# Performance work log

Measured on AMD Instinct MI355X. Metric: run time of the kernel, lower is better.

Reference implementation:

```python
import jax, jax.numpy as jnp
import numpy as np

B, L, D = 32, 256, 128


def hard_sigmoid(x):
    # Keras-1 default inner_activation for LSTM gates
    return jnp.clip(0.2 * x + 0.5, 0.0, 1.0)


def lstm_step(x_t, h, c, W, U, b):
    # Keras-1 gate order: i, f, c(candidate), o
    z = x_t @ W + h @ U + b  # [B, 4D]
    d = h.shape[-1]
    i = hard_sigmoid(z[:, :d])
    f = hard_sigmoid(z[:, d:2 * d])
    g = jnp.tanh(z[:, 2 * d:3 * d])
    o = hard_sigmoid(z[:, 3 * d:])
    c_new = f * c + i * g
    h_new = o * jnp.tanh(c_new)
    return h_new, c_new


def setup_inputs() -> dict:
    key = jax.random.key(0)
    ks = jax.random.split(key, 9)
    s = 0.05  # weight scale to keep activations in a sane range
    return {
        "x": jax.random.normal(ks[0], (B, L, D), dtype=jnp.float32),
        "Wr": jax.random.normal(ks[1], (D, 4 * D), dtype=jnp.float32) * s,
        "Ur": jax.random.normal(ks[2], (D, 4 * D), dtype=jnp.float32) * s,
        "br": jnp.zeros((4 * D,), dtype=jnp.float32),
        "Ww": jax.random.normal(ks[3], (D, 4 * D), dtype=jnp.float32) * s,
        "Uw": jax.random.normal(ks[4], (D, 4 * D), dtype=jnp.float32) * s,
        "bw": jnp.zeros((4 * D,), dtype=jnp.float32),
        "Wc": jax.random.normal(ks[5], (2 * D, D), dtype=jnp.float32) * s,
        "bc": jnp.zeros((D,), dtype=jnp.float32),
    }


def reference(x, Wr, Ur, br, Ww, Uw, bw, Wc, bc):
    b, l, d = x.shape
    h0 = jnp.zeros((b, d), dtype=x.dtype)

    # ---- reader LSTM (return_sequences) ----
    def reader_step(carry, x_t):
        h, c = carry
        h, c = lstm_step(x_t, h, c, Wr, Ur, br)
        return (h, c), h

    _, o_seq = jax.lax.scan(reader_step, (h0, h0), jnp.swapaxes(x, 0, 1))  # [L, B, D]

    # ---- compose-and-write scan over timesteps ----
    mem0 = x  # read() sets mem_0 = input

    def write_step(carry, o_t):
        mem, h, c = carry  # mem: [B, L, D]
        # eq 2-3: attention over memory slots
        z = jax.nn.softmax(jnp.einsum('bd,bld->bl', o_t, mem), axis=-1)  # [B, L]
        m_rt = jnp.einsum('bl,bld->bd', z, mem)  # [B, D]
        # eq 4: composer (linear activation)
        c_t = jnp.concatenate([o_t, m_rt], axis=-1) @ Wc + bc  # [B, D]
        # eq 5: writer LSTM step
        h, c = lstm_step(c_t, h, c, Ww, Uw, bw)
        # eq 6: soft overwrite of memory
        zc = z[:, :, None]
        mem = mem * (1.0 - zc) + h[:, None, :] * zc
        return (mem, h, c), h

    (_, _, _), hs = jax.lax.scan(write_step, (mem0, h0, h0), o_seq)
    # return_mode == 'last_output'
    return hs[-1]
```

## Files before the change

kernel.cpp:

```cpp
#include <hip/hip_runtime.h>
#include <stdint.h>


#define LL 256

typedef float v2f __attribute__((ext_vector_type(2)));

__device__ __forceinline__ float hsig(float x) { return fminf(fmaxf(fmaf(x, 0.2f, 0.5f), 0.f), 1.f); }
__device__ __forceinline__ float tanh_fast(float x) {
  x = fminf(fmaxf(x, -15.f), 15.f);
  float e = __expf(2.f * x);
  return (e - 1.f) / (e + 1.f);
}

__global__ __launch_bounds__(512) void wtrans_kernel(const float* __restrict__ src,
                                                     float* __restrict__ dst, int jshift) {
  int idx = blockIdx.x * 512 + threadIdx.x;
  int J = 1 << jshift;
  int k = idx >> jshift, j = idx & (J - 1);
  dst[(((size_t)(k >> 2) << jshift) + j) * 4 + (k & 3)] = src[idx];
}

__global__ __launch_bounds__(512) void pvw_gemm(const float* __restrict__ Wc,
                                                const float* __restrict__ Ww,
                                                float* __restrict__ PVw) {
  __shared__ float wrow[128];
  const int r = blockIdx.x, j = threadIdx.x;
  if (j < 128) wrow[j] = Wc[r * 128 + j];
  __syncthreads();
  float a = 0.f;
#pragma unroll 4
  for (int m = 0; m < 128; m++) a = fmaf(wrow[m], Ww[m * 512 + j], a);
  PVw[r * 512 + j] = a;
}

__global__ __launch_bounds__(512) void pz_kernel(const float* __restrict__ bc,
                                                 const float* __restrict__ Ww,
                                                 const float* __restrict__ bw,
                                                 float* __restrict__ pz) {
  __shared__ float b_s[128];
  const int j = threadIdx.x;
  if (j < 128) b_s[j] = bc[j];
  __syncthreads();
  float a = bw[j];
#pragma unroll 4
  for (int m = 0; m < 128; m++) a = fmaf(b_s[m], Ww[m * 512 + j], a);
  pz[j] = a;
}

__global__ __launch_bounds__(512) void xw_gemm(const float* __restrict__ x,
                                               const float4* __restrict__ WrT4,
                                               const float* __restrict__ br,
                                               float* __restrict__ XW) {
  alignas(16) __shared__ float xs[8][128];
  const int b = blockIdx.x >> 5, tg = blockIdx.x & 31, tid = threadIdx.x;
  const float* xg = x + ((size_t)b * LL + tg * 8) * 128;
  if (tid < 256) ((float4*)&xs[0][0])[tid] = ((const float4*)xg)[tid];
  __syncthreads();
  float acc[8];
#pragma unroll
  for (int r = 0; r < 8; r++) acc[r] = 0.f;
#pragma unroll 8
  for (int i4 = 0; i4 < 32; i4++) {
    float4 w4 = WrT4[i4 * 512 + tid];
#pragma unroll
    for (int r = 0; r < 8; r++) {
      float4 v = *(const float4*)&xs[r][4 * i4];
      acc[r] += w4.x * v.x + w4.y * v.y + w4.z * v.z + w4.w * v.w;
    }
  }
  const float brj = br[tid];
  float* o = XW + ((size_t)b * LL + tg * 8) * 512;
#pragma unroll
  for (int r = 0; r < 8; r++) o[r * 512 + tid] = acc[r] + brj;
}

__global__ __launch_bounds__(512, 2) void reader_kernel(const float4* __restrict__ UrT4,
                                                        const float* __restrict__ XW,
                                                        float* __restrict__ og) {
  alignas(16) __shared__ float h_s[128];
  alignas(16) __shared__ float pp_s[512];
  const int b = blockIdx.x, tid = threadIdx.x;
  const float* XWb = XW + (size_t)b * LL * 512;
  float* ogb = og + (size_t)b * LL * 128;

  float4 U[32];
#pragma unroll
  for (int i4 = 0; i4 < 32; i4++) U[i4] = UrT4[i4 * 512 + tid];

  float c_r = 0.f;
  if (tid < 128) h_s[tid] = 0.f;
  float xwv = XWb[tid];
  __syncthreads();

  for (int t = 0; t < LL; t++) {
    float xw_n = (t + 1 < LL) ? XWb[(t + 1) * 512 + tid] : 0.f;
    v2f acc[4] = {{0.f, 0.f}, {0.f, 0.f}, {0.f, 0.f}, {0.f, 0.f}};
#pragma unroll
    for (int i4 = 0; i4 < 32; i4++) {
      float4 v = *(const float4*)&h_s[4 * i4];
      float4 w = U[i4];
      acc[i4 & 3] += (v2f){w.x, w.y} * (v2f){v.x, v.y};
      acc[i4 & 3] += (v2f){w.z, w.w} * (v2f){v.z, v.w};
    }
    v2f A = (acc[0] + acc[1]) + (acc[2] + acc[3]);
    pp_s[tid] = A.x + A.y + xwv;
    __syncthreads();
    if (tid < 128) {
      float zi = pp_s[tid], zf = pp_s[128 + tid], zg = pp_s[256 + tid], zo = pp_s[384 + tid];
      float ii = hsig(zi), ff = hsig(zf), gg = tanh_fast(zg), oo = hsig(zo);
      c_r = fmaf(ff, c_r, ii * gg);
      float h = oo * tanh_fast(c_r);
      h_s[tid] = h;
      ogb[t * 128 + tid] = h;
    }
    __syncthreads();
    xwv = xw_n;
  }
}

template <int NC>
__global__ __launch_bounds__(512, 2) void writer_kernel(
    const float* __restrict__ x,
    const float4* __restrict__ VwT4, const float4* __restrict__ UwT4,
    const float* __restrict__ og, const float* __restrict__ ZW,
    float* __restrict__ out) {
  alignas(16) __shared__ float h_s[128];
  alignas(16) __shared__ float osN[128];
  alignas(16) __shared__ float sc_s[256], ee_s[256];
  alignas(16) __shared__ float mr_s[128];
  alignas(16) __shared__ float pp_s[1024];
  __shared__ float rr_s[16];
  extern __shared__ float4 UwL[];

  const int b = blockIdx.x, tid = threadIdx.x;
  const int lane = tid & 63, wv = tid >> 6;
  const int l = tid >> 1, hf = tid & 1;
  const int q = tid >> 6, dp = tid & 63;

  const float* xg = x + (size_t)b * (LL * 128);
  const float* ogb = og + (size_t)b * (LL * 128);
  const float* ZWb = ZW + (size_t)b * (LL * 512);

  for (int i = tid; i < NC * 512; i += 512) UwL[i] = UwT4[i];

  float4 VR[16];
#pragma unroll
  for (int i4 = 0; i4 < 16; i4++) VR[i4] = VwT4[i4 * 512 + tid];

  v2f Mr[32], Mc[32];
#pragma unroll
  for (int w = 0; w < 32; w++) Mr[w] = *(const v2f*)(xg + l * 128 + hf * 64 + 2 * w);
#pragma unroll
  for (int i = 0; i < 32; i++) Mc[i] = *(const v2f*)(xg + (q * 32 + i) * 128 + 2 * dp);

  float c_w = 0.f;
  if (tid < 128) { h_s[tid] = 0.f; osN[tid] = ogb[tid]; }
  __syncthreads();
  {
    v2f S = {0.f, 0.f};
#pragma unroll
    for (int w = 0; w < 32; w++) S += Mr[w] * (*(const v2f*)&osN[hf * 64 + 2 * w]);
    float s = S.x + S.y;
    s += __shfl_xor(s, 1);
    if (hf == 0) sc_s[l] = s;
  }
  __syncthreads();

  float zwv = ZWb[tid];
  for (int t = 0; t < LL; t++) {
    const int tn = (t + 1 < LL) ? t + 1 : t;
    float zw_n = ZWb[(size_t)tn * 512 + tid];

    float huv;
    {
      v2f u0 = {0.f, 0.f}, u1 = {0.f, 0.f}, u2 = {0.f, 0.f}, u3 = {0.f, 0.f};
#pragma unroll 2
      for (int i4 = NC; i4 < 32; i4 += 2) {
        float4 w0 = UwT4[i4 * 512 + tid];
        float4 w1 = UwT4[(i4 + 1) * 512 + tid];
        float4 v0 = *(const float4*)&h_s[4 * i4];
        float4 v1 = *(const float4*)&h_s[4 * i4 + 4];
        u0 += (v2f){w0.x, w0.y} * (v2f){v0.x, v0.y};
        u0 += (v2f){w0.z, w0.w} * (v2f){v0.z, v0.w};
        u1 += (v2f){w1.x, w1.y} * (v2f){v1.x, v1.y};
        u1 += (v2f){w1.z, w1.w} * (v2f){v1.z, v1.w};
      }
#pragma unroll 2
      for (int i4 = 0; i4 < NC; i4++) {
        float4 w = UwL[i4 * 512 + tid];
        float4 v = *(const float4*)&h_s[4 * i4];
        u2 += (v2f){w.x, w.y} * (v2f){v.x, v.y};
        u3 += (v2f){w.z, w.w} * (v2f){v.z, v.w};
      }
      v2f U = (u0 + u1) + (u2 + u3);
      huv = U.x + U.y + zwv;
    }

    if (tid >= 128 && tid < 256 && t + 1 < LL)
      osN[tid - 128] = ogb[(t + 1) * 128 + (tid - 128)];
    if (tid < 256) {
      float s = sc_s[tid];
      float m = s;
#pragma unroll
      for (int off = 32; off > 0; off >>= 1) m = fmaxf(m, __shfl_xor(m, off));
      float e = __expf(s - m);
      ee_s[tid] = e;
      float s2 = e;
#pragma unroll
      for (int off = 32; off > 0; off >>= 1) s2 += __shfl_xor(s2, off);
      if (lane == 0) { rr_s[wv] = m; rr_s[8 + wv] = s2; }
    }
    __syncthreads();

    const float M = fmaxf(fmaxf(rr_s[0], rr_s[1]), fmaxf(rr_s[2], rr_s[3]));
    const float Sg = rr_s[8] * __expf(rr_s[0] - M) + rr_s[9] * __expf(rr_s[1] - M) +
                     rr_s[10] * __expf(rr_s[2] - M) + rr_s[11] * __expf(rr_s[3] - M);
    const float inv = 1.f / Sg;
    const float f = __expf(rr_s[tid >> 7] - M);
    const float fzi = f * inv;

    {
      v2f P0 = {0.f, 0.f}, P1 = {0.f, 0.f};
#pragma unroll
      for (int i = 0; i < 32; i += 2) {
        P0 += Mc[i] * ee_s[q * 32 + i];
        P1 += Mc[i + 1] * ee_s[q * 32 + i + 1];
      }
      v2f P = (P0 + P1) * f;
      *(v2f*)&pp_s[q * 128 + 2 * dp] = P;
    }
    __syncthreads();
    if (tid < 128) {
      float s = 0.f;
#pragma unroll
      for (int g = 0; g < 8; g++) s += pp_s[g * 128 + tid];
      mr_s[tid] = s;
    }
    __syncthreads();
    {
      v2f a0 = {0.f, 0.f}, a1 = {0.f, 0.f}, a2 = {0.f, 0.f}, a3 = {0.f, 0.f};
#pragma unroll 2
      for (int i4 = 16; i4 < 32; i4 += 2) {
        float4 w0 = VwT4[i4 * 512 + tid];
        float4 w1 = VwT4[(i4 + 1) * 512 + tid];
        float4 v0 = *(const float4*)&mr_s[4 * i4];
        float4 v1 = *(const float4*)&mr_s[4 * i4 + 4];
        a0 += (v2f){w0.x, w0.y} * (v2f){v0.x, v0.y};
        a0 += (v2f){w0.z, w0.w} * (v2f){v0.z, v0.w};
        a1 += (v2f){w1.x, w1.y} * (v2f){v1.x, v1.y};
        a1 += (v2f){w1.z, w1.w} * (v2f){v1.z, v1.w};
      }
#pragma unroll
      for (int i4 = 0; i4 < 16; i4 += 2) {
        float4 w0 = VR[i4];
        float4 w1 = VR[i4 + 1];
        float4 v0 = *(const float4*)&mr_s[4 * i4];
        float4 v1 = *(const float4*)&mr_s[4 * i4 + 4];
        a2 += (v2f){w0.x, w0.y} * (v2f){v0.x, v0.y};
        a2 += (v2f){w0.z, w0.w} * (v2f){v0.z, v0.w};
        a3 += (v2f){w1.x, w1.y} * (v2f){v1.x, v1.y};
        a3 += (v2f){w1.z, w1.w} * (v2f){v1.z, v1.w};
      }
      v2f A = (a0 + a2) + (a1 + a3);
      pp_s[tid] = fmaf(A.x + A.y, inv, huv);
    }
    __syncthreads();
    if (tid < 128) {
      float zi = pp_s[tid], zf = pp_s[128 + tid], zg = pp_s[256 + tid], zo = pp_s[384 + tid];
      float ii = hsig(zi), ff = hsig(zf), gg = tanh_fast(zg), oo = hsig(zo);
      c_w = fmaf(ff, c_w, ii * gg);
      h_s[tid] = oo * tanh_fast(c_w);
    }
    __syncthreads();
    if (t + 1 < LL) {
      const float zr = ee_s[l] * fzi;
      v2f S0v = {0.f, 0.f}, S1v = {0.f, 0.f};
#pragma unroll
      for (int w = 0; w < 32; w += 2) {
        v2f h2a = *(const v2f*)&h_s[hf * 64 + 2 * w];
        v2f ma = Mr[w];
        v2f na = ma + (h2a - ma) * zr;
        Mr[w] = na;
        S0v += na * (*(const v2f*)&osN[hf * 64 + 2 * w]);
        v2f h2b = *(const v2f*)&h_s[hf * 64 + 2 * (w + 1)];
        v2f mb = Mr[w + 1];
        v2f nb = mb + (h2b - mb) * zr;
        Mr[w + 1] = nb;
        S1v += nb * (*(const v2f*)&osN[hf * 64 + 2 * (w + 1)]);
      }
      v2f Sv = S0v + S1v;
      float s = Sv.x + Sv.y;
      s += __shfl_xor(s, 1);
      if (hf == 0) sc_s[l] = s;
      v2f hc = *(const v2f*)&h_s[2 * dp];
#pragma unroll
      for (int i = 0; i < 32; i++) {
        float zc = ee_s[q * 32 + i] * fzi;
        v2f m = Mc[i];
        Mc[i] = m + (hc - m) * zc;
      }
    }
    __syncthreads();
    zwv = zw_n;
  }

  if (tid < 128) out[b * 128 + tid] = h_s[tid];
}

extern "C" void kernel_launch(void* const* d_in, const int* in_sizes, int n_in,
                              void* d_out, int out_size, void* d_ws, size_t ws_size,
                              hipStream_t stream) {
  const float* x  = (const float*)d_in[0];
  const float* Wr = (const float*)d_in[1];
  const float* Ur = (const float*)d_in[2];
  const float* br = (const float*)d_in[3];
  const float* Ww = (const float*)d_in[4];
  const float* Uw = (const float*)d_in[5];
  const float* bw = (const float*)d_in[6];
  const float* Wc = (const float*)d_in[7];
  const float* bc = (const float*)d_in[8];
  float* out = (float*)d_out;

  float* og  = (float*)d_ws;
  float* XW  = og + 1048576;
  float* WrT = XW + 4194304;
  float* UrT = WrT + 65536;
  float* UwT = UrT + 65536;
  float* PVw = UwT + 65536;
  float* PwT = PVw + 131072;
  float* VwT = PwT + 65536;
  float* pz  = VwT + 65536;

  static int nc_cached = -1;
  if (nc_cached < 0) {
    int want = 18 * 512 * (int)sizeof(float4);
    nc_cached = (hipFuncSetAttribute(
                     reinterpret_cast<const void*>(&writer_kernel<18>),
                     hipFuncAttributeMaxDynamicSharedMemorySize, want) == hipSuccess)
                    ? 18
                    : 6;
  }

  wtrans_kernel<<<128, 512, 0, stream>>>(Wr, WrT, 9);
  wtrans_kernel<<<128, 512, 0, stream>>>(Ur, UrT, 9);
  wtrans_kernel<<<128, 512, 0, stream>>>(Uw, UwT, 9);
  pvw_gemm<<<256, 512, 0, stream>>>(Wc, Ww, PVw);
  pz_kernel<<<1, 512, 0, stream>>>(bc, Ww, bw, pz);
  wtrans_kernel<<<128, 512, 0, stream>>>(PVw, PwT, 9);
  wtrans_kernel<<<128, 512, 0, stream>>>(PVw + 65536, VwT, 9);
  xw_gemm<<<1024, 512, 0, stream>>>(x, (const float4*)WrT, br, XW);
  reader_kernel<<<32, 512, 0, stream>>>((const float4*)UrT, XW, og);
  xw_gemm<<<1024, 512, 0, stream>>>(og, (const float4*)PwT, pz, XW);
  if (nc_cached == 18) {
    writer_kernel<18><<<32, 512, 18 * 512 * sizeof(float4), stream>>>(
        x, (const float4*)VwT, (const float4*)UwT, og, XW, out);
  } else {
    writer_kernel<6><<<32, 512, 6 * 512 * sizeof(float4), stream>>>(
        x, (const float4*)VwT, (const float4*)UwT, og, XW, out);
  }
}
```

Before: 2.052 ms.

## Remap gate outputs to lane quads, shuffle-combine gates, drop a barrier per step

New measurement: 3.405 ms. +66.0%, slower.

```diff
diff --git a/kernel.cpp b/kernel.cpp
--- a/kernel.cpp
+++ b/kernel.cpp
@@ -137,16 +137,18 @@
   const int lane = tid & 63, wv = tid >> 6;
   const int l = tid >> 1, hf = tid & 1;
   const int q = tid >> 6, dp = tid & 63;
+  const int kk = tid >> 2, g = tid & 3;
+  const int jmap = kk + (g << 7);
+  const int jswz = (kk ^ g) + (g << 7);
 
   const float* xg = x + (size_t)b * (LL * 128);
   const float* ogb = og + (size_t)b * (LL * 128);
   const float* ZWb = ZW + (size_t)b * (LL * 512);
 
-  for (int i = tid; i < NC * 512; i += 512) UwL[i] = UwT4[i];
-
-  float4 VR[16];
-#pragma unroll
-  for (int i4 = 0; i4 < 16; i4++) VR[i4] = VwT4[i4 * 512 + tid];
+  for (int i = tid; i < NC * 512; i += 512) {
+    int i4 = i >> 9, j = i & 511, gj = j >> 7;
+    UwL[(i4 << 9) + (j ^ gj)] = UwT4[i];
+  }
 
   v2f Mr[32], Mc[32];
 #pragma unroll
@@ -167,18 +169,18 @@
   }
   __syncthreads();
 
-  float zwv = ZWb[tid];
+  float zwv = ZWb[jmap];
   for (int t = 0; t < LL; t++) {
     const int tn = (t + 1 < LL) ? t + 1 : t;
-    float zw_n = ZWb[(size_t)tn * 512 + tid];
+    float zw_n = ZWb[(size_t)tn * 512 + jmap];
 
     float huv;
     {
       v2f u0 = {0.f, 0.f}, u1 = {0.f, 0.f}, u2 = {0.f, 0.f}, u3 = {0.f, 0.f};
 #pragma unroll 2
       for (int i4 = NC; i4 < 32; i4 += 2) {
-        float4 w0 = UwT4[i4 * 512 + tid];
-        float4 w1 = UwT4[(i4 + 1) * 512 + tid];
+        float4 w0 = UwT4[i4 * 512 + jmap];
+        float4 w1 = UwT4[(i4 + 1) * 512 + jmap];
         float4 v0 = *(const float4*)&h_s[4 * i4];
         float4 v1 = *(const float4*)&h_s[4 * i4 + 4];
         u0 += (v2f){w0.x, w0.y} * (v2f){v0.x, v0.y};
@@ -188,7 +190,7 @@
       }
 #pragma unroll 2
       for (int i4 = 0; i4 < NC; i4++) {
-        float4 w = UwL[i4 * 512 + tid];
+        float4 w = UwL[(i4 << 9) + jswz];
         float4 v = *(const float4*)&h_s[4 * i4];
         u2 += (v2f){w.x, w.y} * (v2f){v.x, v.y};
         u3 += (v2f){w.z, w.w} * (v2f){v.z, v.w};
@@ -196,6 +198,11 @@
       v2f U = (u0 + u1) + (u2 + u3);
       huv = U.x + U.y + zwv;
     }
+
+    float4 pf0 = VwT4[0 * 512 + jmap], pf1 = VwT4[1 * 512 + jmap];
+    float4 pf2 = VwT4[2 * 512 + jmap], pf3 = VwT4[3 * 512 + jmap];
+    float4 pf4 = VwT4[4 * 512 + jmap], pf5 = VwT4[5 * 512 + jmap];
+    float4 pf6 = VwT4[6 * 512 + jmap], pf7 = VwT4[7 * 512 + jmap];
 
     if (tid >= 128 && tid < 256 && t + 1 < LL)
       osN[tid - 128] = ogb[(t + 1) * 128 + (tid - 128)];
@@ -234,16 +241,16 @@
     if (tid < 128) {
       float s = 0.f;
 #pragma unroll
-      for (int g = 0; g < 8; g++) s += pp_s[g * 128 + tid];
+      for (int g8 = 0; g8 < 8; g8++) s += pp_s[g8 * 128 + tid];
       mr_s[tid] = s;
     }
     __syncthreads();
     {
       v2f a0 = {0.f, 0.f}, a1 = {0.f, 0.f}, a2 = {0.f, 0.f}, a3 = {0.f, 0.f};
 #pragma unroll 2
-      for (int i4 = 16; i4 < 32; i4 += 2) {
-        float4 w0 = VwT4[i4 * 512 + tid];
-        float4 w1 = VwT4[(i4 + 1) * 512 + tid];
+      for (int i4 = 8; i4 < 32; i4 += 2) {
+        float4 w0 = VwT4[i4 * 512 + jmap];
+        float4 w1 = VwT4[(i4 + 1) * 512 + jmap];
         float4 v0 = *(const float4*)&mr_s[4 * i4];
         float4 v1 = *(const float4*)&mr_s[4 * i4 + 4];
         a0 += (v2f){w0.x, w0.y} * (v2f){v0.x, v0.y};
@@ -251,26 +258,33 @@
         a1 += (v2f){w1.x, w1.y} * (v2f){v1.x, v1.y};
         a1 += (v2f){w1.z, w1.w} * (v2f){v1.z, v1.w};
       }
-#pragma unroll
-      for (int i4 = 0; i4 < 16; i4 += 2) {
-        float4 w0 = VR[i4];
-        float4 w1 = VR[i4 + 1];
-        float4 v0 = *(const float4*)&mr_s[4 * i4];
-        float4 v1 = *(const float4*)&mr_s[4 * i4 + 4];
-        a2 += (v2f){w0.x, w0.y} * (v2f){v0.x, v0.y};
-        a2 += (v2f){w0.z, w0.w} * (v2f){v0.z, v0.w};
-        a3 += (v2f){w1.x, w1.y} * (v2f){v1.x, v1.y};
-        a3 += (v2f){w1.z, w1.w} * (v2f){v1.z, v1.w};
+      {
+        float4 m0 = *(const float4*)&mr_s[0],  m1 = *(const float4*)&mr_s[4];
+        float4 m2 = *(const float4*)&mr_s[8],  m3 = *(const float4*)&mr_s[12];
+        float4 m4 = *(const float4*)&mr_s[16], m5 = *(const float4*)&mr_s[20];
+        float4 m6 = *(const float4*)&mr_s[24], m7 = *(const float4*)&mr_s[28];
+        a2 += (v2f){pf0.x, pf0.y} * (v2f){m0.x, m0.y}; a2 += (v2f){pf0.z, pf0.w} * (v2f){m0.z, m0.w};
+        a3 += (v2f){pf1.x, pf1.y} * (v2f){m1.x, m1.y}; a3 += (v2f){pf1.z, pf1.w} * (v2f){m1.z, m1.w};
+        a2 += (v2f){pf2.x, pf2.y} * (v2f){m2.x, m2.y}; a2 += (v2f){pf2.z, pf2.w} * (v2f){m2.z, m2.w};
+        a3 += (v2f){pf3.x, pf3.y} * (v2f){m3.x, m3.y}; a3 += (v2f){pf3.z, pf3.w} * (v2f){m3.z, m3.w};
+        a2 += (v2f){pf4.x, pf4.y} * (v2f){m4.x, m4.y}; a2 += (v2f){pf4.z, pf4.w} * (v2f){m4.z, m4.w};
+        a3 += (v2f){pf5.x, pf5.y} * (v2f){m5.x, m5.y}; a3 += (v2f){pf5.z, pf5.w} * (v2f){m5.z, m5.w};
+        a2 += (v2f){pf6.x, pf6.y} * (v2f){m6.x, m6.y}; a2 += (v2f){pf6.z, pf6.w} * (v2f){m6.z, m6.w};
+        a3 += (v2f){pf7.x, pf7.y} * (v2f){m7.x, m7.y}; a3 += (v2f){pf7.z, pf7.w} * (v2f){m7.z, m7.w};
       }
       v2f A = (a0 + a2) + (a1 + a3);
-      pp_s[tid] = fmaf(A.x + A.y, inv, huv);
-    }
-    __syncthreads();
-    if (tid < 128) {
-      float zi = pp_s[tid], zf = pp_s[128 + tid], zg = pp_s[256 + tid], zo = pp_s[384 + tid];
-      float ii = hsig(zi), ff = hsig(zf), gg = tanh_fast(zg), oo = hsig(zo);
-      c_w = fmaf(ff, c_w, ii * gg);
-      h_s[tid] = oo * tanh_fast(c_w);
+      float zv = fmaf(A.x + A.y, inv, huv);
+      float sv1 = __shfl_xor(zv, 1);
+      float sv2 = __shfl_xor(zv, 2);
+      float sv3 = __shfl_xor(sv1, 2);
+      float zi = (g == 0) ? zv : (g == 1) ? sv1 : (g == 2) ? sv2 : sv3;
+      float zf = (g == 1) ? zv : (g == 0) ? sv1 : (g == 3) ? sv2 : sv3;
+      float zg = (g == 2) ? zv : (g == 3) ? sv1 : (g == 0) ? sv2 : sv3;
+      float zo = (g == 3) ? zv : (g == 2) ? sv1 : (g == 1) ? sv2 : sv3;
+      float ii = hsig(zi), ff = hsig(zf), gg2 = tanh_fast(zg), oo = hsig(zo);
+      c_w = fmaf(ff, c_w, ii * gg2);
+      float hh = oo * tanh_fast(c_w);
+      if (g == 0) h_s[kk] = hh;
     }
     __syncthreads();
     if (t + 1 < LL) {
```
